# Kernel optimization log

Hardware: AMD Instinct MI355X
Metric: run time of the kernel (lower is better)

## Reference

```python
import jax, jax.numpy as jnp
import numpy as np

D_MODEL = 1024
M = 4
NUM_EXPERTS = 8
TOP_K = 2
B, T = 2, 2048


def setup_inputs() -> dict:
    key = jax.random.key(0)
    ks = jax.random.split(key, 4)
    d_ff = D_MODEL * M
    x = jax.random.normal(ks[0], (B, T, D_MODEL), dtype=jnp.float32)
    # torch nn.Linear(d_model, num_experts, bias=False): stored here as (D, E) so logits = x @ gate_w
    gate_w = jax.random.normal(ks[1], (D_MODEL, NUM_EXPERTS), dtype=jnp.float32) * 0.02
    w1 = jax.random.normal(ks[2], (NUM_EXPERTS, D_MODEL, d_ff), dtype=jnp.float32) * 0.02
    b1 = jnp.zeros((NUM_EXPERTS, d_ff), dtype=jnp.float32)
    w2 = jax.random.normal(ks[3], (NUM_EXPERTS, d_ff, D_MODEL), dtype=jnp.float32) * 0.02
    b2 = jnp.zeros((NUM_EXPERTS, D_MODEL), dtype=jnp.float32)
    return {"x": x, "gate_w": gate_w, "w1": w1, "b1": b1, "w2": w2, "b2": b2}


def reference(x, gate_w, w1, b1, w2, b2):
    Bb, Tt, D = x.shape
    E = w1.shape[0]
    N = Bb * Tt
    # gating: top-k logits -> softmax over the k selected experts
    logits = jnp.einsum('btd,de->bte', x, gate_w)               # (B,T,E)
    top_v, top_i = jax.lax.top_k(logits, TOP_K)                 # (B,T,K)
    top_w = jax.nn.softmax(top_v, axis=-1)                      # (B,T,K)

    xf = x.reshape(N, D)
    idx = top_i.reshape(N, TOP_K)
    wts = top_w.reshape(N, TOP_K)
    # dense combine weights: comb[n, e] = sum_k wts[n,k] * [idx[n,k]==e]
    comb = jnp.zeros((N, E), dtype=x.dtype).at[jnp.arange(N)[:, None], idx].add(wts)

    # per-expert dense 2-layer MLP (exact erf GELU, matching torch F.gelu default),
    # combined with gate weights (zero weight == token not routed to expert).
    out = jnp.zeros((N, D), dtype=x.dtype)
    for e in range(E):
        h = jax.nn.gelu(xf @ w1[e] + b1[e], approximate=False)  # (N, D*M)
        out = out + comb[:, e:e + 1] * (h @ w2[e] + b2[e])      # (N, D)
    return out.reshape(Bb, Tt, D)
```

## Files before the change

### kernel.cpp

```cpp
#include <hip/hip_runtime.h>
#include <hip/hip_bf16.h>
#include <math.h>

#define D_MODEL 1024
#define D_FF    4096
#define NEXP    8
#define NTOK    4096
#define NROUTED 8192
#define MAXJOBS 40

typedef __attribute__((ext_vector_type(8))) short bf16x8;
typedef __attribute__((ext_vector_type(4))) float f32x4;
typedef __attribute__((ext_vector_type(4))) unsigned short us4;

#define WS_CNT   0
#define WS_CNT2  64
#define WS_OFF   128
#define WS_JOBS  192
#define WS_TI    512
#define WS_TW    (WS_TI + NTOK*2*4)
#define WS_TOK   (WS_TW + NTOK*2*4)
#define WS_GWT   (WS_TOK + NROUTED*4)
#define WS_XG    (((WS_GWT + NROUTED*4) + 255) & ~255)
#define WS_H     (WS_XG + (size_t)NROUTED*D_MODEL*2)
#define WS_WT    (WS_H + (size_t)NROUTED*D_FF*2)

__device__ __forceinline__ unsigned short f2bf(float f){
  union { float f; unsigned u; } a; a.f = f;
  unsigned u = a.u;
  u = u + 0x7FFF + ((u >> 16) & 1);
  return (unsigned short)(u >> 16);
}

__device__ __forceinline__ void gload_lds16(const void* g, void* l){
  __builtin_amdgcn_global_load_lds((const __attribute__((address_space(1))) void*)g,
                                   (__attribute__((address_space(3))) void*)l, 16, 0, 0);
}

__global__ void moe_gate_kernel(const float* __restrict__ x, const float* __restrict__ gw,
                                int* cnt, int* __restrict__ ti, float* __restrict__ tw){
  int n = blockIdx.x*4 + (threadIdx.x >> 6);
  int lane = threadIdx.x & 63;
  const float* xr = x + (size_t)n * D_MODEL;
  float acc[NEXP];
  #pragma unroll
  for (int e=0;e<NEXP;e++) acc[e] = 0.f;
  for (int d=lane; d<D_MODEL; d+=64){
    float xv = xr[d];
    #pragma unroll
    for (int e=0;e<NEXP;e++) acc[e] += xv * gw[d*NEXP + e];
  }
  #pragma unroll
  for (int e=0;e<NEXP;e++){
    #pragma unroll
    for (int o=32;o;o>>=1) acc[e] += __shfl_down(acc[e], o, 64);
  }
  if (lane == 0){
    int i0 = 0; float v0 = acc[0];
    #pragma unroll
    for (int e=1;e<NEXP;e++) if (acc[e] > v0){ v0 = acc[e]; i0 = e; }
    int i1 = -1; float v1 = -1e30f;
    #pragma unroll
    for (int e=0;e<NEXP;e++) if (e != i0 && acc[e] > v1){ v1 = acc[e]; i1 = e; }
    float p = expf(v1 - v0);
    float inv = 1.f / (1.f + p);
    ti[n*2] = i0; ti[n*2+1] = i1;
    tw[n*2] = inv; tw[n*2+1] = p * inv;
    atomicAdd(&cnt[i0], 1); atomicAdd(&cnt[i1], 1);
  }
}

__global__ void moe_prefix_kernel(const int* __restrict__ cnt, int* __restrict__ off,
                                  int* __restrict__ jobs){
  if (threadIdx.x == 0){
    int s = 0;
    for (int e=0;e<NEXP;e++){ off[e] = s; s += cnt[e]; }
    off[NEXP] = s;
    int idx = 0;
    for (int e=0;e<NEXP;e++){
      int ns = (cnt[e] + 255) >> 8;
      for (int q=0;q<ns;q++) jobs[1+idx++] = (e<<16) | q;
    }
    jobs[0] = idx;
  }
}

__global__ void moe_assign_kernel(const float* __restrict__ x, const int* __restrict__ ti,
                                  const float* __restrict__ tw, const int* __restrict__ off,
                                  int* cnt2, int* __restrict__ tok, float* __restrict__ gwt,
                                  unsigned short* __restrict__ Xg){
  __shared__ int ss[2];
  int n = blockIdx.x;
  if (threadIdx.x == 0){
    int i0 = ti[n*2], i1 = ti[n*2+1];
    int s0 = off[i0] + atomicAdd(&cnt2[i0], 1);
    int s1 = off[i1] + atomicAdd(&cnt2[i1], 1);
    tok[s0] = n; tok[s1] = n;
    gwt[s0] = tw[n*2]; gwt[s1] = tw[n*2+1];
    ss[0] = s0; ss[1] = s1;
  }
  __syncthreads();
  int s0 = ss[0], s1 = ss[1];
  int t = threadIdx.x;
  float4 v = ((const float4*)(x + (size_t)n * D_MODEL))[t];
  us4 pk = { f2bf(v.x), f2bf(v.y), f2bf(v.z), f2bf(v.w) };
  *(us4*)(Xg + (size_t)s0 * D_MODEL + t*4) = pk;
  *(us4*)(Xg + (size_t)s1 * D_MODEL + t*4) = pk;
}

__global__ __launch_bounds__(256) void transpose_bf16_kernel(
    const float* __restrict__ W, unsigned short* __restrict__ Wt, int K, int F){
  __shared__ float tile[64][65];
  int e = blockIdx.z;
  int f0 = blockIdx.x * 64, k0 = blockIdx.y * 64;
  const float* Wb = W + (size_t)e * K * F;
  unsigned short* Wtb = Wt + (size_t)e * F * K;
  int tid = threadIdx.x;
  #pragma unroll
  for (int i=0;i<4;i++){
    int idx = i*256 + tid;
    int r = idx >> 4, c4 = (idx & 15) * 4;
    float4 v = *(const float4*)(Wb + (size_t)(k0 + r) * F + f0 + c4);
    tile[r][c4] = v.x; tile[r][c4+1] = v.y; tile[r][c4+2] = v.z; tile[r][c4+3] = v.w;
  }
  __syncthreads();
  #pragma unroll
  for (int i=0;i<4;i++){
    int idx = i*256 + tid;
    int f = idx >> 4, k4 = (idx & 15) * 4;
    us4 pk = { f2bf(tile[k4][f]), f2bf(tile[k4+1][f]), f2bf(tile[k4+2][f]), f2bf(tile[k4+3][f]) };
    *(us4*)(Wtb + (size_t)(f0 + f) * K + k0 + k4) = pk;
  }
}

template<int MODE>
__global__ __launch_bounds__(1024) void moe_gemm_kernel(
    char* __restrict__ wsb, const unsigned short* __restrict__ Bt,
    const float* __restrict__ bias, float* __restrict__ out)
{
  const int* jobs = (const int*)(wsb + WS_JOBS);
  if ((int)blockIdx.y >= jobs[0]) return;
  const int jb = jobs[1 + blockIdx.y];
  const int e = jb >> 16;
  const int row0 = (jb & 0xffff) << 8;

  const int* off = (const int*)(wsb + WS_OFF);
  const int n0 = off[e];
  const int ne = off[e+1] - n0;

  constexpr int K  = (MODE==1) ? D_MODEL : D_FF;
  constexpr int NT = 32;
  const int bx     = (MODE==1) ? blockIdx.x : (blockIdx.x & 3);
  const int kchunk = (MODE==1) ? 0 : (blockIdx.x >> 2);
  const int n_off  = bx * 256;
  const size_t kcb = (size_t)kchunk * 2048;

  const unsigned short* Ag  = (const unsigned short*)(wsb + (MODE==1 ? (size_t)WS_XG : (size_t)WS_H));
  const unsigned short* Bgt = Bt + (size_t)e * D_FF * D_MODEL;

  __shared__ __align__(16) char lds[3*32768];

  const int tid = threadIdx.x, lane = tid & 63, w = tid >> 6;
  const int wr = w >> 2, wc = w & 3;

  const int rA   = w*16 + (lane >> 2);
  const int qs   = ((lane & 3) ^ ((rA >> 1) & 3)) << 4;
  int grA = row0 + rA; if (grA >= ne) grA = ne - 1;
  const char* aSrc = (const char*)(Ag + (size_t)(n0 + grA) * K) + kcb + qs;
  const char* bSrc = (const char*)(Bgt + (size_t)(n_off + rA) * K) + kcb + qs;
  const int dA = w*1024, dB = 16384 + w*1024;

  const int q0 = lane >> 4;
  int aoff[4], boff[4];
  #pragma unroll
  for (int mi=0; mi<4; mi++){
    int row = wr*64 + mi*16 + (lane & 15);
    aoff[mi] = row*64 + ((q0 ^ ((row>>1)&3)) << 4);
  }
  #pragma unroll
  for (int ni=0; ni<4; ni++){
    int col = wc*64 + ni*16 + (lane & 15);
    boff[ni] = 16384 + col*64 + ((q0 ^ ((col>>1)&3)) << 4);
  }

  f32x4 acc[4][4];
  #pragma unroll
  for (int i=0;i<4;i++)
    #pragma unroll
    for (int j=0;j<4;j++) acc[i][j] = (f32x4){0.f,0.f,0.f,0.f};

  #define STAGE(tt, ss) { \
    gload_lds16(aSrc + (size_t)(tt)*64, lds + (ss)*32768 + dA); \
    gload_lds16(bSrc + (size_t)(tt)*64, lds + (ss)*32768 + dB); }

  STAGE(0, 0);
  STAGE(1, 1);

  for (int t = 0; t < NT; ++t){
    if (t < NT-1) asm volatile("s_waitcnt vmcnt(2)" ::: "memory");
    else          asm volatile("s_waitcnt vmcnt(0)" ::: "memory");
    __builtin_amdgcn_s_barrier();
    __builtin_amdgcn_sched_barrier(0);

    if (t + 2 < NT) STAGE(t + 2, (t + 2) % 3);

    const char* base = lds + (t % 3) * 32768;
    bf16x8 a[4], b[4];
    #pragma unroll
    for (int mi=0; mi<4; mi++) a[mi] = *(const bf16x8*)(base + aoff[mi]);
    #pragma unroll
    for (int ni=0; ni<4; ni++) b[ni] = *(const bf16x8*)(base + boff[ni]);

    asm volatile("s_waitcnt lgkmcnt(0)" ::: "memory");
    __builtin_amdgcn_sched_barrier(0);
    __builtin_amdgcn_s_setprio(1);
    #pragma unroll
    for (int ni=0; ni<4; ni++)
      #pragma unroll
      for (int mi=0; mi<4; mi++)
        acc[mi][ni] = __builtin_amdgcn_mfma_f32_16x16x32_bf16(a[mi], b[ni], acc[mi][ni], 0, 0, 0);
    __builtin_amdgcn_s_setprio(0);
    __builtin_amdgcn_sched_barrier(0);
  }
  #undef STAGE

  if (MODE == 1){
    const float* b1 = bias + (size_t)e * D_FF;
    unsigned short* H = (unsigned short*)(wsb + (size_t)WS_H);
    #pragma unroll
    for (int mi=0; mi<4; mi++){
      int rbase = wr*64 + mi*16 + ((lane>>4)<<2);
      #pragma unroll
      for (int rr=0;rr<4;rr++){
        int lrow = rbase + rr;
        if (row0 + lrow < ne){
          size_t hb = (size_t)(n0 + row0 + lrow) * D_FF;
          #pragma unroll
          for (int ni=0; ni<4; ni++){
            int gcol = n_off + wc*64 + ni*16 + (lane&15);
            float v = acc[mi][ni][rr] + b1[gcol];
            v = 0.5f * v * (1.f + erff(v * 0.70710678118654752f));
            H[hb + gcol] = f2bf(v);
          }
        }
      }
    }
  } else {
    const float* b2 = bias + (size_t)e * D_MODEL;
    const int* tok = (const int*)(wsb + WS_TOK);
    const float* gwt = (const float*)(wsb + WS_GWT);
    #pragma unroll
    for (int mi=0; mi<4; mi++){
      int rbase = wr*64 + mi*16 + ((lane>>4)<<2);
      #pragma unroll
      for (int rr=0;rr<4;rr++){
        int lrow = rbase + rr;
        if (row0 + lrow < ne){
          int slot = n0 + row0 + lrow;
          int tk = tok[slot];
          float g = gwt[slot];
          float* orow = out + (size_t)tk * D_MODEL;
          #pragma unroll
          for (int ni=0; ni<4; ni++){
            int gcol = n_off + wc*64 + ni*16 + (lane&15);
            float bb = (kchunk == 0) ? b2[gcol] : 0.f;
            atomicAdd(orow + gcol, (acc[mi][ni][rr] + bb) * g);
          }
        }
      }
    }
  }
}

extern "C" void kernel_launch(void* const* d_in, const int* in_sizes, int n_in,
                              void* d_out, int out_size, void* d_ws, size_t ws_size,
                              hipStream_t stream){
  const float* x   = (const float*)d_in[0];
  const float* gw  = (const float*)d_in[1];
  const float* w1  = (const float*)d_in[2];
  const float* b1  = (const float*)d_in[3];
  const float* w2  = (const float*)d_in[4];
  const float* b2  = (const float*)d_in[5];
  float* out = (float*)d_out;
  char* ws = (char*)d_ws;
  unsigned short* Wt = (unsigned short*)(ws + (size_t)WS_WT);

  hipMemsetAsync(ws, 0, 512, stream);
  hipMemsetAsync(out, 0, (size_t)NTOK * D_MODEL * sizeof(float), stream);

  moe_gate_kernel<<<NTOK/4, 256, 0, stream>>>(x, gw, (int*)(ws+WS_CNT),
                                              (int*)(ws+WS_TI), (float*)(ws+WS_TW));
  moe_prefix_kernel<<<1, 64, 0, stream>>>((const int*)(ws+WS_CNT), (int*)(ws+WS_OFF),
                                          (int*)(ws+WS_JOBS));
  moe_assign_kernel<<<NTOK, 256, 0, stream>>>(x, (const int*)(ws+WS_TI),
                                              (const float*)(ws+WS_TW), (const int*)(ws+WS_OFF),
                                              (int*)(ws+WS_CNT2), (int*)(ws+WS_TOK),
                                              (float*)(ws+WS_GWT),
                                              (unsigned short*)(ws + (size_t)WS_XG));
  transpose_bf16_kernel<<<dim3(D_FF/64, D_MODEL/64, NEXP), 256, 0, stream>>>(w1, Wt, D_MODEL, D_FF);
  moe_gemm_kernel<1><<<dim3(D_FF/256, MAXJOBS), 1024, 0, stream>>>(ws, Wt, b1, out);
  transpose_bf16_kernel<<<dim3(D_MODEL/64, D_FF/64, NEXP), 256, 0, stream>>>(w2, Wt, D_FF, D_MODEL);
  moe_gemm_kernel<2><<<dim3((D_MODEL/256)*4, MAXJOBS), 1024, 0, stream>>>(ws, Wt, b2, out);
}
```

Measured before the change: 593.1 us.

## Restructure MoE GEMM to 512 threads, BK=128, double-buffered 8x4 MFMA tiles

Moves the expert GEMM kernel from 1024 threads with a 3-stage BK=64 pipeline to 512 threads with a 2-stage BK=128 pipeline. Each wave now computes 128x64 of output (8x4 MFMA tiles) instead of 64x64, which raises register reuse of loaded fragments and halves the number of barriers per K. It also switches to an XOR-by-row 128-byte LDS swizzle. In exchange it uses 128 KB of LDS per block, which may limit occupancy despite the (512,2) launch bound, and it drops the setprio/sched_barrier hints and the deeper prefetch.

```diff
diff --git a/kernel.cpp b/kernel.cpp
--- a/kernel.cpp
+++ b/kernel.cpp
@@ -134,7 +134,7 @@
 }
 
 template<int MODE>
-__global__ __launch_bounds__(1024) void moe_gemm_kernel(
+__global__ __launch_bounds__(512, 2) void moe_gemm_kernel(
     char* __restrict__ wsb, const unsigned short* __restrict__ Bt,
     const float* __restrict__ bias, float* __restrict__ out)
 {
@@ -149,7 +149,7 @@
   const int ne = off[e+1] - n0;
 
   constexpr int K  = (MODE==1) ? D_MODEL : D_FF;
-  constexpr int NT = 32;
+  constexpr int NT = 16;
   const int bx     = (MODE==1) ? blockIdx.x : (blockIdx.x & 3);
   const int kchunk = (MODE==1) ? 0 : (blockIdx.x >> 2);
   const int n_off  = bx * 256;
@@ -158,69 +158,71 @@
   const unsigned short* Ag  = (const unsigned short*)(wsb + (MODE==1 ? (size_t)WS_XG : (size_t)WS_H));
   const unsigned short* Bgt = Bt + (size_t)e * D_FF * D_MODEL;
 
-  __shared__ __align__(16) char lds[3*32768];
+  __shared__ __align__(16) char lds[2*65536];
 
   const int tid = threadIdx.x, lane = tid & 63, w = tid >> 6;
   const int wr = w >> 2, wc = w & 3;
 
-  const int rA   = w*16 + (lane >> 2);
-  const int qs   = ((lane & 3) ^ ((rA >> 1) & 3)) << 4;
-  int grA = row0 + rA; if (grA >= ne) grA = ne - 1;
-  const char* aSrc = (const char*)(Ag + (size_t)(n0 + grA) * K) + kcb + qs;
-  const char* bSrc = (const char*)(Bgt + (size_t)(n_off + rA) * K) + kcb + qs;
-  const int dA = w*1024, dB = 16384 + w*1024;
-
-  const int q0 = lane >> 4;
-  int aoff[4], boff[4];
-  #pragma unroll
-  for (int mi=0; mi<4; mi++){
-    int row = wr*64 + mi*16 + (lane & 15);
-    aoff[mi] = row*64 + ((q0 ^ ((row>>1)&3)) << 4);
-  }
-  #pragma unroll
-  for (int ni=0; ni<4; ni++){
-    int col = wc*64 + ni*16 + (lane & 15);
-    boff[ni] = 16384 + col*64 + ((q0 ^ ((col>>1)&3)) << 4);
-  }
-
-  f32x4 acc[4][4];
-  #pragma unroll
-  for (int i=0;i<4;i++)
+  const int arow   = lane >> 3;
+  const int achunk = ((lane & 7) ^ arow) << 4;
+  const char* aP[4]; const char* bP[4];
+  #pragma unroll
+  for (int i=0;i<4;i++){
+    int r = (w*4 + i)*8 + arow;
+    int gr = row0 + r; if (gr >= ne) gr = ne - 1;
+    aP[i] = (const char*)(Ag + (size_t)(n0 + gr) * K) + kcb + achunk;
+    bP[i] = (const char*)(Bgt + (size_t)(n_off + r) * K) + kcb + achunk;
+  }
+  const int dstA = w*4096;
+
+  f32x4 acc[8][4];
+  #pragma unroll
+  for (int i=0;i<8;i++)
     #pragma unroll
     for (int j=0;j<4;j++) acc[i][j] = (f32x4){0.f,0.f,0.f,0.f};
 
-  #define STAGE(tt, ss) { \
-    gload_lds16(aSrc + (size_t)(tt)*64, lds + (ss)*32768 + dA); \
-    gload_lds16(bSrc + (size_t)(tt)*64, lds + (ss)*32768 + dB); }
+  #define STAGE(tt, bb) { \
+    size_t kb = (size_t)(tt)*128; \
+    char* d = lds + (bb)*65536 + dstA; \
+    _Pragma("unroll") \
+    for (int i=0;i<4;i++){ \
+      gload_lds16(aP[i] + kb, d + i*1024); \
+      gload_lds16(bP[i] + kb, d + 32768 + i*1024); \
+    } }
 
   STAGE(0, 0);
-  STAGE(1, 1);
-
+  asm volatile("s_waitcnt vmcnt(0)" ::: "memory");
+  __builtin_amdgcn_s_barrier();
+
+  int cur = 0;
   for (int t = 0; t < NT; ++t){
-    if (t < NT-1) asm volatile("s_waitcnt vmcnt(2)" ::: "memory");
-    else          asm volatile("s_waitcnt vmcnt(0)" ::: "memory");
+    if (t + 1 < NT) STAGE(t + 1, cur ^ 1);
+
+    const char* base = lds + cur*65536;
+    const int q16 = (lane >> 4) << 4;
+    #pragma unroll
+    for (int kk=0; kk<2; ++kk){
+      bf16x8 a[8], b[4];
+      #pragma unroll
+      for (int mi=0; mi<8; mi++){
+        int row = wr*128 + mi*16 + (lane&15);
+        a[mi] = *(const bf16x8*)(base + (row<<7) + (((kk<<6) + q16) ^ ((row&7)<<4)));
+      }
+      #pragma unroll
+      for (int ni=0; ni<4; ni++){
+        int col = wc*64 + ni*16 + (lane&15);
+        b[ni] = *(const bf16x8*)(base + 32768 + (col<<7) + (((kk<<6) + q16) ^ ((col&7)<<4)));
+      }
+      #pragma unroll
+      for (int ni=0; ni<4; ni++)
+        #pragma unroll
+        for (int mi=0; mi<8; mi++)
+          acc[mi][ni] = __builtin_amdgcn_mfma_f32_16x16x32_bf16(a[mi], b[ni], acc[mi][ni], 0, 0, 0);
+    }
+
+    if (t + 1 < NT) asm volatile("s_waitcnt vmcnt(0)" ::: "memory");
     __builtin_amdgcn_s_barrier();
-    __builtin_amdgcn_sched_barrier(0);
-
-    if (t + 2 < NT) STAGE(t + 2, (t + 2) % 3);
-
-    const char* base = lds + (t % 3) * 32768;
-    bf16x8 a[4], b[4];
-    #pragma unroll
-    for (int mi=0; mi<4; mi++) a[mi] = *(const bf16x8*)(base + aoff[mi]);
-    #pragma unroll
-    for (int ni=0; ni<4; ni++) b[ni] = *(const bf16x8*)(base + boff[ni]);
-
-    asm volatile("s_waitcnt lgkmcnt(0)" ::: "memory");
-    __builtin_amdgcn_sched_barrier(0);
-    __builtin_amdgcn_s_setprio(1);
-    #pragma unroll
-    for (int ni=0; ni<4; ni++)
-      #pragma unroll
-      for (int mi=0; mi<4; mi++)
-        acc[mi][ni] = __builtin_amdgcn_mfma_f32_16x16x32_bf16(a[mi], b[ni], acc[mi][ni], 0, 0, 0);
-    __builtin_amdgcn_s_setprio(0);
-    __builtin_amdgcn_sched_barrier(0);
+    cur ^= 1;
   }
   #undef STAGE
 
@@ -228,8 +230,8 @@
     const float* b1 = bias + (size_t)e * D_FF;
     unsigned short* H = (unsigned short*)(wsb + (size_t)WS_H);
     #pragma unroll
-    for (int mi=0; mi<4; mi++){
-      int rbase = wr*64 + mi*16 + ((lane>>4)<<2);
+    for (int mi=0; mi<8; mi++){
+      int rbase = wr*128 + mi*16 + ((lane>>4)<<2);
       #pragma unroll
       for (int rr=0;rr<4;rr++){
         int lrow = rbase + rr;
@@ -250,8 +252,8 @@
     const int* tok = (const int*)(wsb + WS_TOK);
     const float* gwt = (const float*)(wsb + WS_GWT);
     #pragma unroll
-    for (int mi=0; mi<4; mi++){
-      int rbase = wr*64 + mi*16 + ((lane>>4)<<2);
+    for (int mi=0; mi<8; mi++){
+      int rbase = wr*128 + mi*16 + ((lane>>4)<<2);
       #pragma unroll
       for (int rr=0;rr<4;rr++){
         int lrow = rbase + rr;
@@ -298,7 +300,7 @@
                                               (float*)(ws+WS_GWT),
                                               (unsigned short*)(ws + (size_t)WS_XG));
   transpose_bf16_kernel<<<dim3(D_FF/64, D_MODEL/64, NEXP), 256, 0, stream>>>(w1, Wt, D_MODEL, D_FF);
-  moe_gemm_kernel<1><<<dim3(D_FF/256, MAXJOBS), 1024, 0, stream>>>(ws, Wt, b1, out);
+  moe_gemm_kernel<1><<<dim3(D_FF/256, MAXJOBS), 512, 0, stream>>>(ws, Wt, b1, out);
   transpose_bf16_kernel<<<dim3(D_MODEL/64, D_FF/64, NEXP), 256, 0, stream>>>(w2, Wt, D_FF, D_MODEL);
-  moe_gemm_kernel<2><<<dim3((D_MODEL/256)*4, MAXJOBS), 1024, 0, stream>>>(ws, Wt, b2, out);
-}
+  moe_gemm_kernel<2><<<dim3((D_MODEL/256)*4, MAXJOBS), 512, 0, stream>>>(ws, Wt, b2, out);
+}
```

Result: slower. 645.7 us (+8.9%).
